# Kernel tuning notes

Hardware: AMD Instinct MI355X
Metric: run time of the kernel (lower is better)

Reference implementation:

```python
import jax, jax.numpy as jnp
import numpy as np

DIM = 1536
NUM_HEADS = 24
HEAD_DIM = DIM // NUM_HEADS
SCALE = HEAD_DIM ** -0.5
B, NX, NC = 2, 2048, 256


def setup_inputs() -> dict:
    key = jax.random.key(0)
    ks = jax.random.split(key, 12)
    s = 0.02
    return {
        "x": jax.random.normal(ks[0], (B, NX, DIM), jnp.float32),
        "c": jax.random.normal(ks[1], (B, NC, DIM), jnp.float32),
        "Wqkv_x": jax.random.normal(ks[2], (3 * DIM, DIM), jnp.float32) * s,
        "bqkv_x": jax.random.normal(ks[3], (3 * DIM,), jnp.float32) * s,
        "Wqkv_c": jax.random.normal(ks[4], (3 * DIM, DIM), jnp.float32) * s,
        "bqkv_c": jax.random.normal(ks[5], (3 * DIM,), jnp.float32) * s,
        "Wproj_x": jax.random.normal(ks[6], (DIM, DIM), jnp.float32) * s,
        "bproj_x": jax.random.normal(ks[7], (DIM,), jnp.float32) * s,
        "Wproj_c": jax.random.normal(ks[8], (DIM, DIM), jnp.float32) * s,
        "bproj_c": jax.random.normal(ks[9], (DIM,), jnp.float32) * s,
    }


def _qkv(t, W, b):
    # t: [B, N, C] -> q, k, v each [B, H, N, Dh]
    Bt, N, C = t.shape
    qkv = (t @ W.T + b).reshape(Bt, N, 3, NUM_HEADS, HEAD_DIM)
    qkv = jnp.transpose(qkv, (2, 0, 3, 1, 4))  # [3, B, H, N, Dh]
    return qkv[0], qkv[1], qkv[2]


def reference(x, c, Wqkv_x, bqkv_x, Wqkv_c, bqkv_c, Wproj_x, bproj_x, Wproj_c, bproj_c):
    q_x, k_x, v_x = _qkv(x, Wqkv_x, bqkv_x)
    q_c, k_c, v_c = _qkv(c, Wqkv_c, bqkv_c)
    q = jnp.concatenate([q_x, q_c], axis=2)  # [B, H, Nx+Nc, Dh]
    k = jnp.concatenate([k_x, k_c], axis=2)
    v = jnp.concatenate([v_x, v_c], axis=2)
    attn = jnp.einsum("bhnd,bhmd->bhnm", q, k) * SCALE
    attn = jax.nn.softmax(attn, axis=-1)
    out = jnp.einsum("bhnm,bhmd->bhnd", attn, v)  # [B, H, N, Dh]
    x_out = out[:, :, :NX]
    c_out = out[:, :, NX:]
    x_out = jnp.transpose(x_out, (0, 2, 1, 3)).reshape(x.shape[0], NX, DIM)
    c_out = jnp.transpose(c_out, (0, 2, 1, 3)).reshape(c.shape[0], NC, DIM)
    return (x_out @ Wproj_x.T + bproj_x, c_out @ Wproj_c.T + bproj_c)
```

## Files before the change

kernel.cpp:

```cpp
#include <hip/hip_runtime.h>
#include <stdint.h>

#define HNUM 24
#define DIMX 1536
#define NXT  2048
#define NCT  256
#define NTOT 2304
#define BB   2
#define NK   (DIMX / 64)

typedef __attribute__((ext_vector_type(8))) short bf16x8;
typedef __attribute__((ext_vector_type(8))) _Float16 f16x8;
typedef __attribute__((ext_vector_type(4))) _Float16 f16x4;
typedef __attribute__((ext_vector_type(2))) _Float16 f16x2;
typedef __attribute__((ext_vector_type(2))) __fp16 hp16x2;
typedef __attribute__((ext_vector_type(4))) float f32x4;
typedef __attribute__((ext_vector_type(4))) unsigned short u16x4;

#define AS1 __attribute__((address_space(1)))
#define AS3 __attribute__((address_space(3)))

__device__ __forceinline__ void glds16(const void* g, void* l) {
  __builtin_amdgcn_global_load_lds((AS1 void*)(uintptr_t)g, (AS3 void*)l, 16, 0, 0);
}

__device__ __forceinline__ unsigned short f2bf(float f) {
  unsigned int u = __float_as_uint(f);
  u += 0x7FFFu + ((u >> 16) & 1u);
  return (unsigned short)(u >> 16);
}

__device__ __forceinline__ f16x2 pkrtz(float a, float b) {
  hp16x2 r = __builtin_amdgcn_cvt_pkrtz(a, b);
  union { hp16x2 h; f16x2 f; } u;
  u.h = r;
  return u.f;
}

__device__ __forceinline__ bf16x8 ldfragB(const unsigned short* S, int row, int cc) {
  return *(const bf16x8*)(S + row * 64 + ((cc ^ (row & 7)) << 3));
}
__device__ __forceinline__ f16x8 ldVfrag8(const _Float16* S, int row, int mbp, int quad) {
  int cc = (quad * 2 + mbp) ^ (row & 7);
  return *(const f16x8*)(S + row * 64 + cc * 8);
}

struct CastDesc { const float* src; unsigned short* dst; int start4; };
struct CastArgs { CastDesc d[6]; int total4; };

__global__ __launch_bounds__(256) void cast_all(CastArgs a) {
  int i = blockIdx.x * 256 + threadIdx.x;
  if (i >= a.total4) return;
  int r = 0;
#pragma unroll
  for (int k = 1; k < 6; ++k) r += (i >= a.d[k].start4);
  int j = i - a.d[r].start4;
  float4 v = reinterpret_cast<const float4*>(a.d[r].src)[j];
  u16x4 o;
  o[0] = f2bf(v.x); o[1] = f2bf(v.y); o[2] = f2bf(v.z); o[3] = f2bf(v.w);
  reinterpret_cast<u16x4*>(a.d[r].dst)[j] = o;
}

__device__ __forceinline__ void gemm_mainloop256(
    const unsigned short* __restrict__ Ablk,
    const unsigned short* __restrict__ Wblk,
    unsigned short* As, unsigned short* Bs, f32x4 acc[4][4]) {
  const int tid  = threadIdx.x;
  const int lane = tid & 63;
  const int quad = lane >> 4, l16 = lane & 15;
  const int wave = tid >> 6;
  const int wm = (wave >> 1) * 64, wo = (wave & 1) * 64;

  auto stageA = [&](int kt, int buf, int i) {
    int c = i * 512 + tid;
    int row = c >> 3;
    int kc = ((c & 7) ^ (row & 7)) << 3;
    glds16(Ablk + (size_t)row * DIMX + kt * 64 + kc, As + buf * (256 * 64) + c * 8);
  };
  auto stageB = [&](int kt, int buf, int i) {
    int c = i * 512 + tid;
    int row = c >> 3;
    int kc = ((c & 7) ^ (row & 7)) << 3;
    glds16(Wblk + (size_t)row * DIMX + kt * 64 + kc, Bs + buf * (128 * 64) + c * 8);
  };

  stageA(0, 0, 0); stageA(0, 0, 1); stageA(0, 0, 2); stageA(0, 0, 3);
  stageB(0, 0, 0); stageB(0, 0, 1);
  stageA(1, 1, 0); stageA(1, 1, 1); stageA(1, 1, 2); stageA(1, 1, 3);
  stageB(1, 1, 0); stageB(1, 1, 1);
  asm volatile("s_waitcnt vmcnt(6)" ::: "memory");
  __builtin_amdgcn_s_barrier();

  int cur = 0;
  for (int kt = 0; kt < NK; ++kt) {
    const unsigned short* A_ = As + cur * (256 * 64);
    const unsigned short* B_ = Bs + cur * (128 * 64);
    const int stg = (cur == 0) ? 2 : cur - 1;
    const bool doStage = (kt + 2 < NK);
#pragma unroll
    for (int kk = 0; kk < 2; ++kk) {
      bf16x8 af[4], bfr[4];
#pragma unroll
      for (int mb = 0; mb < 4; ++mb)
        af[mb] = ldfragB(A_, wm + mb * 16 + l16, kk * 4 + quad);
#pragma unroll
      for (int ob = 0; ob < 4; ++ob)
        bfr[ob] = ldfragB(B_, wo + ob * 16 + l16, kk * 4 + quad);
      if (doStage) {
        if (kk == 0) { stageA(kt + 2, stg, 0); stageA(kt + 2, stg, 1); stageA(kt + 2, stg, 2); }
        else         { stageA(kt + 2, stg, 3); stageB(kt + 2, stg, 0); stageB(kt + 2, stg, 1); }
      }
      __builtin_amdgcn_s_setprio(1);
#pragma unroll
      for (int mb = 0; mb < 4; ++mb)
#pragma unroll
        for (int ob = 0; ob < 4; ++ob)
          acc[mb][ob] = __builtin_amdgcn_mfma_f32_16x16x32_bf16(
              af[mb], bfr[ob], acc[mb][ob], 0, 0, 0);
      __builtin_amdgcn_s_setprio(0);
    }
    if (doStage)          asm volatile("s_waitcnt vmcnt(6)" ::: "memory");
    else if (kt + 1 < NK) asm volatile("s_waitcnt vmcnt(0)" ::: "memory");
    __builtin_amdgcn_s_barrier();
    cur = (cur == 2) ? 0 : cur + 1;
  }
}

__global__ __launch_bounds__(512, 2) void gemm_qkv(
    const unsigned short* __restrict__ xbf, const unsigned short* __restrict__ cbf,
    const unsigned short* __restrict__ Wx, const unsigned short* __restrict__ Wc,
    const float* __restrict__ bx_, const float* __restrict__ bc_,
    unsigned short* __restrict__ Qb, unsigned short* __restrict__ Kb,
    _Float16* __restrict__ VTf) {
  __shared__ unsigned short SA[3][256 * 64];
  __shared__ unsigned short SB[3][128 * 64];

  const int swz = ((int)blockIdx.x & 7) * (648 / 8) + ((int)blockIdx.x >> 3);
  const int bx = swz % 36;
  const int by = swz / 36;

  const bool isC = by >= 16;
  const int yloc = isC ? by - 16 : by;
  const int tokShift = isC ? 8 : 11;
  const int seqOff = isC ? NXT : 0;
  const unsigned short* A = (isC ? cbf : xbf) + (size_t)yloc * 256 * DIMX;
  const unsigned short* W = (isC ? Wc : Wx) + (size_t)bx * 128 * DIMX;
  const float* bias = isC ? bc_ : bx_;

  const f32x4 z4 = {0.f, 0.f, 0.f, 0.f};
  f32x4 acc[4][4];
#pragma unroll
  for (int i = 0; i < 4; ++i)
#pragma unroll
    for (int j = 0; j < 4; ++j) acc[i][j] = z4;

  gemm_mainloop256(A, W, &SA[0][0], &SB[0][0], acc);

  const int tid = threadIdx.x, lane = tid & 63, wave = tid >> 6;
  const int quad = lane >> 4, l16 = lane & 15;
  const int wm = (wave >> 1) * 64, wo = (wave & 1) * 64;
  const int s = bx / 12;
  const float QSC = 0.125f * 1.44269504088896340736f;

  float bv[4];
#pragma unroll
  for (int ob = 0; ob < 4; ++ob)
    bv[ob] = bias[bx * 128 + wo + ob * 16 + l16];

  if (s < 2) {
#pragma unroll
    for (int ob = 0; ob < 4; ++ob) {
      int o = bx * 128 + wo + ob * 16 + l16;
      int rem = o - s * DIMX;
      int h = rem >> 6, d = rem & 63;
#pragma unroll
      for (int mb = 0; mb < 4; ++mb) {
#pragma unroll
        for (int r = 0; r < 4; ++r) {
          int m = yloc * 256 + wm + mb * 16 + quad * 4 + r;
          int b = m >> tokShift;
          int n = seqOff + (m & ((1 << tokShift) - 1));
          size_t bh = (size_t)b * HNUM + h;
          float v = acc[mb][ob][r] + bv[ob];
          if (s == 0) Qb[(bh * NTOT + n) * 64 + d] = f2bf(v * QSC);
          else        Kb[(bh * NTOT + n) * 64 + d] = f2bf(v);
        }
      }
    }
  } else {
    _Float16* Ts = (_Float16*)SA;
    __syncthreads();
#pragma unroll
    for (int ob = 0; ob < 4; ++ob) {
      int dloc = wo + ob * 16 + l16;
      int sw = (dloc & 31) << 3;
#pragma unroll
      for (int mb = 0; mb < 4; ++mb) {
        f16x4 pk;
#pragma unroll
        for (int r = 0; r < 4; ++r) pk[r] = (_Float16)(acc[mb][ob][r] + bv[ob]);
        int m0 = wm + mb * 16 + quad * 4;
        *(f16x4*)(Ts + dloc * 256 + (m0 ^ sw)) = pk;
      }
    }
    __syncthreads();
#pragma unroll
    for (int it = 0; it < 8; ++it) {
      int cth = it * 512 + tid;
      int d = cth >> 5;
      int m0 = (cth & 31) << 3;
      f16x8 val = *(const f16x8*)(Ts + d * 256 + (m0 ^ ((d & 31) << 3)));
      int dglob = (bx - 24) * 128 + d;
      int h = dglob >> 6, dd = dglob & 63;
      int M = yloc * 256 + m0;
      int b = M >> tokShift;
      int n = seqOff + (M & ((1 << tokShift) - 1));
      *(f16x8*)(VTf + ((size_t)(b * HNUM + h) * 64 + dd) * NTOT + n) = val;
    }
  }
}

__global__ __launch_bounds__(512, 2) void gemm_proj(
    const unsigned short* __restrict__ AX, const unsigned short* __restrict__ AC,
    const unsigned short* __restrict__ Wx, const unsigned short* __restrict__ Wc,
    const float* __restrict__ bx_, const float* __restrict__ bc_,
    float* __restrict__ out) {
  __shared__ unsigned short SA[3][256 * 64];
  __shared__ unsigned short SB[3][128 * 64];

  const int swz = ((int)blockIdx.x & 7) * (216 / 8) + ((int)blockIdx.x >> 3);
  const int bx = swz % 12;
  const int by = swz / 12;

  const bool isC = by >= 16;
  const int yloc = isC ? by - 16 : by;
  const unsigned short* A = (isC ? AC : AX) + (size_t)yloc * 256 * DIMX;
  const unsigned short* W = (isC ? Wc : Wx) + (size_t)bx * 128 * DIMX;
  const float* bias = isC ? bc_ : bx_;
  float* o_ = out + (isC ? (size_t)BB * NXT * DIMX : (size_t)0) +
              (size_t)yloc * 256 * DIMX;

  const f32x4 z4 = {0.f, 0.f, 0.f, 0.f};
  f32x4 acc[4][4];
#pragma unroll
  for (int i = 0; i < 4; ++i)
#pragma unroll
    for (int j = 0; j < 4; ++j) acc[i][j] = z4;

  gemm_mainloop256(A, W, &SA[0][0], &SB[0][0], acc);

  const int lane = threadIdx.x & 63, wave = threadIdx.x >> 6;
  const int quad = lane >> 4, l16 = lane & 15;
  const int wm = (wave >> 1) * 64, wo = (wave & 1) * 64;

#pragma unroll
  for (int ob = 0; ob < 4; ++ob) {
    int o = bx * 128 + wo + ob * 16 + l16;
    float bv = bias[o];
#pragma unroll
    for (int mb = 0; mb < 4; ++mb) {
#pragma unroll
      for (int r = 0; r < 4; ++r) {
        int m = wm + mb * 16 + quad * 4 + r;
        o_[(size_t)m * DIMX + o] = acc[mb][ob][r] + bv;
      }
    }
  }
}

__global__ __launch_bounds__(512, 4) void flash_attn(
    const unsigned short* __restrict__ Qb, const unsigned short* __restrict__ Kb,
    const _Float16* __restrict__ Vf,
    unsigned short* __restrict__ AX, unsigned short* __restrict__ AC) {
  __shared__ unsigned short Ks[2][64 * 64];
  __shared__ _Float16      Vs[2][64 * 64];

  const int tid = threadIdx.x, lane = tid & 63, wave = tid >> 6;
  const int quad = lane >> 4, l16 = lane & 15;
  const int bh = blockIdx.y;
  const int qbase = blockIdx.x * 256 + wave * 32;

  bf16x8 qf[2][2];
#pragma unroll
  for (int qb = 0; qb < 2; ++qb)
#pragma unroll
    for (int kh = 0; kh < 2; ++kh)
      qf[qb][kh] = *(const bf16x8*)(
          Qb + ((size_t)bh * NTOT + qbase + qb * 16 + l16) * 64 + kh * 32 + quad * 8);

  const f32x4 z4 = {0.f, 0.f, 0.f, 0.f};
  f32x4 accT[2][4];
  f32x4 lacc[2];
#pragma unroll
  for (int qb = 0; qb < 2; ++qb) {
    lacc[qb] = z4;
#pragma unroll
    for (int db = 0; db < 4; ++db) accT[qb][db] = z4;
  }

  const size_t kbase = (size_t)bh * NTOT * 64;
  const size_t vbase = (size_t)bh * 64 * NTOT;
  const f16x4 ones4 = {(_Float16)1.f, (_Float16)1.f, (_Float16)1.f, (_Float16)1.f};

  const int srow = tid >> 3, scc = tid & 7;
  const int squad = scc >> 1, smbp = scc & 1;
  const int skv = 32 * smbp + squad * 4;
  _Float16* const sdst0 = &Vs[0][0] + srow * 64 + ((scc ^ (srow & 7)) << 3);
  _Float16* const sdst1 = &Vs[1][0] + srow * 64 + ((scc ^ (srow & 7)) << 3);
  const _Float16* const vsrc = Vf + vbase + (size_t)srow * NTOT + skv;

  f16x4 vstg0, vstg1;
  auto loadV = [&](int kt) {
    vstg0 = *(const f16x4*)(vsrc + kt * 64);
    vstg1 = *(const f16x4*)(vsrc + kt * 64 + 16);
  };
  auto writeV = [&](int kt) {
    f16x8 w;
    w[0] = vstg0[0]; w[1] = vstg0[1]; w[2] = vstg0[2]; w[3] = vstg0[3];
    w[4] = vstg1[0]; w[5] = vstg1[1]; w[6] = vstg1[2]; w[7] = vstg1[3];
    *(f16x8*)((kt & 1) ? sdst1 : sdst0) = w;
  };
  auto stageK = [&](int kt) {
    const int kv0 = kt * 64;
    int row = tid >> 3;
    int kc = ((tid & 7) ^ (row & 7)) << 3;
    glds16(Kb + kbase + (size_t)(kv0 + row) * 64 + kc, &Ks[kt & 1][0] + tid * 8);
  };

  loadV(0);
  stageK(0);
  writeV(0);
  for (int kt = 0; kt < 36; ++kt) {
    __syncthreads();
    if (kt < 35) { loadV(kt + 1); stageK(kt + 1); }
    const unsigned short* K_ = &Ks[kt & 1][0];
    const _Float16*       V_ = &Vs[kt & 1][0];

    f32x4 st[2][4];
#pragma unroll
    for (int qb = 0; qb < 2; ++qb)
#pragma unroll
      for (int mb = 0; mb < 4; ++mb) st[qb][mb] = z4;
    __builtin_amdgcn_s_setprio(1);
#pragma unroll
    for (int kh = 0; kh < 2; ++kh) {
#pragma unroll
      for (int mb = 0; mb < 4; ++mb) {
        bf16x8 kf = ldfragB(K_, mb * 16 + l16, kh * 4 + quad);
#pragma unroll
        for (int qb = 0; qb < 2; ++qb)
          st[qb][mb] = __builtin_amdgcn_mfma_f32_16x16x32_bf16(
              kf, qf[qb][kh], st[qb][mb], 0, 0, 0);
      }
    }
    __builtin_amdgcn_s_setprio(0);

    f16x4 pf[2][4];
#pragma unroll
    for (int qb = 0; qb < 2; ++qb) {
#pragma unroll
      for (int mb = 0; mb < 4; ++mb) {
        float p0 = __builtin_amdgcn_exp2f(st[qb][mb][0]);
        float p1 = __builtin_amdgcn_exp2f(st[qb][mb][1]);
        float p2 = __builtin_amdgcn_exp2f(st[qb][mb][2]);
        float p3 = __builtin_amdgcn_exp2f(st[qb][mb][3]);
        f16x2 lo = pkrtz(p0, p1);
        f16x2 hi = pkrtz(p2, p3);
        f16x4 pk = {lo[0], lo[1], hi[0], hi[1]};
        pf[qb][mb] = pk;
        lacc[qb] = __builtin_amdgcn_mfma_f32_16x16x16f16(
            ones4, pk, lacc[qb], 0, 0, 0);
      }
    }

    if (kt < 35) writeV(kt + 1);

    __builtin_amdgcn_s_setprio(1);
#pragma unroll
    for (int db = 0; db < 4; ++db) {
#pragma unroll
      for (int mbp = 0; mbp < 2; ++mbp) {
        f16x8 v2 = ldVfrag8(V_, db * 16 + l16, mbp, quad);
        f16x4 vlo = {v2[0], v2[1], v2[2], v2[3]};
        f16x4 vhi = {v2[4], v2[5], v2[6], v2[7]};
#pragma unroll
        for (int qb = 0; qb < 2; ++qb)
          accT[qb][db] = __builtin_amdgcn_mfma_f32_16x16x16f16(
              vlo, pf[qb][2 * mbp], accT[qb][db], 0, 0, 0);
#pragma unroll
        for (int qb = 0; qb < 2; ++qb)
          accT[qb][db] = __builtin_amdgcn_mfma_f32_16x16x16f16(
              vhi, pf[qb][2 * mbp + 1], accT[qb][db], 0, 0, 0);
      }
    }
    __builtin_amdgcn_s_setprio(0);
  }

  float inv[2];
#pragma unroll
  for (int qb = 0; qb < 2; ++qb) inv[qb] = __frcp_rn(lacc[qb][0]);

  const int b = bh / HNUM, h = bh - b * HNUM;
#pragma unroll
  for (int qb = 0; qb < 2; ++qb) {
    int n = qbase + qb * 16 + l16;
#pragma unroll
    for (int db = 0; db < 4; ++db) {
      u16x4 o;
#pragma unroll
      for (int r = 0; r < 4; ++r) o[r] = f2bf(accT[qb][db][r] * inv[qb]);
      int col = h * 64 + db * 16 + quad * 4;
      if (n < NXT)
        *(u16x4*)(AX + ((size_t)b * NXT + n) * DIMX + col) = o;
      else
        *(u16x4*)(AC + ((size_t)b * NCT + (n - NXT)) * DIMX + col) = o;
    }
  }
}

extern "C" void kernel_launch(void* const* d_in, const int* in_sizes, int n_in,
                              void* d_out, int out_size, void* d_ws, size_t ws_size,
                              hipStream_t stream) {
  const float* x       = (const float*)d_in[0];
  const float* c       = (const float*)d_in[1];
  const float* Wqkv_x  = (const float*)d_in[2];
  const float* bqkv_x  = (const float*)d_in[3];
  const float* Wqkv_c  = (const float*)d_in[4];
  const float* bqkv_c  = (const float*)d_in[5];
  const float* Wproj_x = (const float*)d_in[6];
  const float* bproj_x = (const float*)d_in[7];
  const float* Wproj_c = (const float*)d_in[8];
  const float* bproj_c = (const float*)d_in[9];
  float* out = (float*)d_out;

  char* ws = (char*)d_ws;
  size_t off = 0;
  auto alloc = [&](size_t nelem) {
    unsigned short* p = (unsigned short*)(ws + off);
    off += nelem * 2;
    return p;
  };
  unsigned short* xbf  = alloc((size_t)BB * NXT * DIMX);
  unsigned short* cbf  = alloc((size_t)BB * NCT * DIMX);
  unsigned short* wqx  = alloc((size_t)3 * DIMX * DIMX);
  unsigned short* wqc  = alloc((size_t)3 * DIMX * DIMX);
  unsigned short* wpx  = alloc((size_t)DIMX * DIMX);
  unsigned short* wpc  = alloc((size_t)DIMX * DIMX);
  unsigned short* Qb   = alloc((size_t)BB * HNUM * NTOT * 64);
  unsigned short* Kb   = alloc((size_t)BB * HNUM * NTOT * 64);
  _Float16*       VTf  = (_Float16*)alloc((size_t)BB * HNUM * NTOT * 64);
  unsigned short* AX   = alloc((size_t)BB * NXT * DIMX);
  unsigned short* AC   = alloc((size_t)BB * NCT * DIMX);

  CastArgs ca;
  const float* srcs[6] = {x, c, Wqkv_x, Wqkv_c, Wproj_x, Wproj_c};
  unsigned short* dsts[6] = {xbf, cbf, wqx, wqc, wpx, wpc};
  size_t ns[6] = {(size_t)BB * NXT * DIMX, (size_t)BB * NCT * DIMX,
                  (size_t)3 * DIMX * DIMX, (size_t)3 * DIMX * DIMX,
                  (size_t)DIMX * DIMX, (size_t)DIMX * DIMX};
  int acc4 = 0;
  for (int i = 0; i < 6; ++i) {
    ca.d[i].src = srcs[i];
    ca.d[i].dst = dsts[i];
    ca.d[i].start4 = acc4;
    acc4 += (int)(ns[i] / 4);
  }
  ca.total4 = acc4;
  cast_all<<<dim3((acc4 + 255) / 256), dim3(256), 0, stream>>>(ca);

  gemm_qkv<<<dim3(648), dim3(512), 0, stream>>>(xbf, cbf, wqx, wqc,
                                                bqkv_x, bqkv_c, Qb, Kb, VTf);

  flash_attn<<<dim3(9, 48), dim3(512), 0, stream>>>(Qb, Kb, VTf, AX, AC);

  gemm_proj<<<dim3(216), dim3(512), 0, stream>>>(AX, AC, wpx, wpc,
                                                 bproj_x, bproj_c, out);
}
```

Baseline: 339.9 us.

## Use 32x32x16 MFMA for PV and compute row sums with fdot2

Replaces the P·V product, previously 32 16x16x16 f16 MFMAs per tile, with 8 32x32x16 MFMAs. P fragments are rebuilt through cross-lane shuffles to fit the larger B-operand layout, and V staging becomes a single 16-byte load per thread. The softmax row sums move off the MFMA unit to VALU fdot2 accumulation with a final cross-lane reduction, and the output write is remapped to the 32x32 accumulator layout. The aim is fewer MFMA issues and less matrix-pipe pressure, at the cost of extra shuffles and VALU work per tile.

```diff
diff --git a/kernel.cpp b/kernel.cpp
--- a/kernel.cpp
+++ b/kernel.cpp
@@ -15,6 +15,7 @@
 typedef __attribute__((ext_vector_type(2))) _Float16 f16x2;
 typedef __attribute__((ext_vector_type(2))) __fp16 hp16x2;
 typedef __attribute__((ext_vector_type(4))) float f32x4;
+typedef __attribute__((ext_vector_type(16))) float f32x16;
 typedef __attribute__((ext_vector_type(4))) unsigned short u16x4;
 
 #define AS1 __attribute__((address_space(1)))
@@ -40,9 +41,9 @@
 __device__ __forceinline__ bf16x8 ldfragB(const unsigned short* S, int row, int cc) {
   return *(const bf16x8*)(S + row * 64 + ((cc ^ (row & 7)) << 3));
 }
-__device__ __forceinline__ f16x8 ldVfrag8(const _Float16* S, int row, int mbp, int quad) {
-  int cc = (quad * 2 + mbp) ^ (row & 7);
-  return *(const f16x8*)(S + row * 64 + cc * 8);
+__device__ __forceinline__ f16x8 ldV32(const _Float16* S, int row, int w, int hi32) {
+  int c = (w * 2 + hi32) ^ (row & 7);
+  return *(const f16x8*)(S + row * 64 + c * 8);
 }
 
 struct CastDesc { const float* src; unsigned short* dst; int start4; };
@@ -277,6 +278,7 @@
 
   const int tid = threadIdx.x, lane = tid & 63, wave = tid >> 6;
   const int quad = lane >> 4, l16 = lane & 15;
+  const int l31 = lane & 31, hi32 = lane >> 5;
   const int bh = blockIdx.y;
   const int qbase = blockIdx.x * 256 + wave * 32;
 
@@ -289,37 +291,25 @@
           Qb + ((size_t)bh * NTOT + qbase + qb * 16 + l16) * 64 + kh * 32 + quad * 8);
 
   const f32x4 z4 = {0.f, 0.f, 0.f, 0.f};
-  f32x4 accT[2][4];
-  f32x4 lacc[2];
-#pragma unroll
-  for (int qb = 0; qb < 2; ++qb) {
-    lacc[qb] = z4;
-#pragma unroll
-    for (int db = 0; db < 4; ++db) accT[qb][db] = z4;
-  }
+  f32x16 accT[2];
+#pragma unroll
+  for (int db = 0; db < 2; ++db)
+#pragma unroll
+    for (int r = 0; r < 16; ++r) accT[db][r] = 0.f;
+  float lp[2] = {0.f, 0.f};
 
   const size_t kbase = (size_t)bh * NTOT * 64;
   const size_t vbase = (size_t)bh * 64 * NTOT;
-  const f16x4 ones4 = {(_Float16)1.f, (_Float16)1.f, (_Float16)1.f, (_Float16)1.f};
+  const f16x2 one2 = {(_Float16)1.f, (_Float16)1.f};
 
   const int srow = tid >> 3, scc = tid & 7;
-  const int squad = scc >> 1, smbp = scc & 1;
-  const int skv = 32 * smbp + squad * 4;
   _Float16* const sdst0 = &Vs[0][0] + srow * 64 + ((scc ^ (srow & 7)) << 3);
   _Float16* const sdst1 = &Vs[1][0] + srow * 64 + ((scc ^ (srow & 7)) << 3);
-  const _Float16* const vsrc = Vf + vbase + (size_t)srow * NTOT + skv;
-
-  f16x4 vstg0, vstg1;
-  auto loadV = [&](int kt) {
-    vstg0 = *(const f16x4*)(vsrc + kt * 64);
-    vstg1 = *(const f16x4*)(vsrc + kt * 64 + 16);
-  };
-  auto writeV = [&](int kt) {
-    f16x8 w;
-    w[0] = vstg0[0]; w[1] = vstg0[1]; w[2] = vstg0[2]; w[3] = vstg0[3];
-    w[4] = vstg1[0]; w[5] = vstg1[1]; w[6] = vstg1[2]; w[7] = vstg1[3];
-    *(f16x8*)((kt & 1) ? sdst1 : sdst0) = w;
-  };
+  const _Float16* const vsrc = Vf + vbase + (size_t)srow * NTOT + scc * 8;
+
+  f16x8 vstg;
+  auto loadV = [&](int kt) { vstg = *(const f16x8*)(vsrc + (size_t)kt * 64); };
+  auto writeV = [&](int kt) { *(f16x8*)((kt & 1) ? sdst1 : sdst0) = vstg; };
   auto stageK = [&](int kt) {
     const int kv0 = kt * 64;
     int row = tid >> 3;
@@ -366,31 +356,41 @@
         float p3 = __builtin_amdgcn_exp2f(st[qb][mb][3]);
         f16x2 lo = pkrtz(p0, p1);
         f16x2 hi = pkrtz(p2, p3);
+        lp[qb] = __builtin_amdgcn_fdot2(lo, one2, lp[qb], false);
+        lp[qb] = __builtin_amdgcn_fdot2(hi, one2, lp[qb], false);
         f16x4 pk = {lo[0], lo[1], hi[0], hi[1]};
         pf[qb][mb] = pk;
-        lacc[qb] = __builtin_amdgcn_mfma_f32_16x16x16f16(
-            ones4, pk, lacc[qb], 0, 0, 0);
-      }
+      }
+    }
+
+    f16x8 bfr[4];
+    const bool loQ = (lane & 16) != 0;
+#pragma unroll
+    for (int mb = 0; mb < 4; ++mb) {
+      union { f16x4 v; unsigned int u[2]; } pk_, ps_;
+      pk_.v = loQ ? pf[1][mb] : pf[0][mb];
+      ps_.v = loQ ? pf[0][mb] : pf[1][mb];
+      unsigned int rec0 = (unsigned int)__shfl_xor((int)ps_.u[0], 16);
+      unsigned int rec1 = (unsigned int)__shfl_xor((int)ps_.u[1], 16);
+      union { f16x8 v; unsigned int u[4]; } bb;
+      bb.u[0] = loQ ? rec0 : pk_.u[0];
+      bb.u[1] = loQ ? rec1 : pk_.u[1];
+      bb.u[2] = loQ ? pk_.u[0] : rec0;
+      bb.u[3] = loQ ? pk_.u[1] : rec1;
+      bfr[mb] = bb.v;
     }
 
     if (kt < 35) writeV(kt + 1);
 
     __builtin_amdgcn_s_setprio(1);
 #pragma unroll
-    for (int db = 0; db < 4; ++db) {
-#pragma unroll
-      for (int mbp = 0; mbp < 2; ++mbp) {
-        f16x8 v2 = ldVfrag8(V_, db * 16 + l16, mbp, quad);
-        f16x4 vlo = {v2[0], v2[1], v2[2], v2[3]};
-        f16x4 vhi = {v2[4], v2[5], v2[6], v2[7]};
-#pragma unroll
-        for (int qb = 0; qb < 2; ++qb)
-          accT[qb][db] = __builtin_amdgcn_mfma_f32_16x16x16f16(
-              vlo, pf[qb][2 * mbp], accT[qb][db], 0, 0, 0);
-#pragma unroll
-        for (int qb = 0; qb < 2; ++qb)
-          accT[qb][db] = __builtin_amdgcn_mfma_f32_16x16x16f16(
-              vhi, pf[qb][2 * mbp + 1], accT[qb][db], 0, 0, 0);
+    for (int db = 0; db < 2; ++db) {
+      const int vrow = db * 32 + l31;
+#pragma unroll
+      for (int w = 0; w < 4; ++w) {
+        f16x8 va = ldV32(V_, vrow, w, hi32);
+        accT[db] = __builtin_amdgcn_mfma_f32_32x32x16_f16(
+            va, bfr[w], accT[db], 0, 0, 0);
       }
     }
     __builtin_amdgcn_s_setprio(0);
@@ -398,22 +398,30 @@
 
   float inv[2];
 #pragma unroll
-  for (int qb = 0; qb < 2; ++qb) inv[qb] = __frcp_rn(lacc[qb][0]);
+  for (int qb = 0; qb < 2; ++qb) {
+    float l = lp[qb];
+    l += __shfl_xor(l, 16);
+    l += __shfl_xor(l, 32);
+    inv[qb] = __frcp_rn(l);
+  }
+  const float invSel = (lane & 16) ? inv[1] : inv[0];
 
   const int b = bh / HNUM, h = bh - b * HNUM;
-#pragma unroll
-  for (int qb = 0; qb < 2; ++qb) {
-    int n = qbase + qb * 16 + l16;
-#pragma unroll
-    for (int db = 0; db < 4; ++db) {
-      u16x4 o;
-#pragma unroll
-      for (int r = 0; r < 4; ++r) o[r] = f2bf(accT[qb][db][r] * inv[qb]);
-      int col = h * 64 + db * 16 + quad * 4;
-      if (n < NXT)
-        *(u16x4*)(AX + ((size_t)b * NXT + n) * DIMX + col) = o;
-      else
-        *(u16x4*)(AC + ((size_t)b * NCT + (n - NXT)) * DIMX + col) = o;
+  {
+    int n = qbase + l31;
+#pragma unroll
+    for (int db = 0; db < 2; ++db) {
+#pragma unroll
+      for (int rq = 0; rq < 4; ++rq) {
+        u16x4 o;
+#pragma unroll
+        for (int r = 0; r < 4; ++r) o[r] = f2bf(accT[db][rq * 4 + r] * invSel);
+        int col = h * 64 + db * 32 + rq * 8 + hi32 * 4;
+        if (n < NXT)
+          *(u16x4*)(AX + ((size_t)b * NXT + n) * DIMX + col) = o;
+        else
+          *(u16x4*)(AC + ((size_t)b * NCT + (n - NXT)) * DIMX + col) = o;
+      }
     }
   }
 }
```

Measured after the change: 352.3 us. +3.6%, slower.
